# Kernel optimization log

Measured on AMD Instinct MI355X. Metric: run time of the kernel, lower is better.

Reference implementation:

```python
import jax, jax.numpy as jnp
import numpy as np

PERIOD = 64
SCALE = 0.45


def setup_inputs() -> dict:
    key = jax.random.key(0)
    kq, kk, kv = jax.random.split(key, 3)
    B, L, D = 16, 8192, 512
    q = jax.random.normal(kq, (B, L, D), dtype=jnp.float32)
    k = jax.random.normal(kk, (B, L, D), dtype=jnp.float32)
    v = jax.random.normal(kv, (B, L, D), dtype=jnp.float32)
    return {"q": q, "k": k, "v": v}


def reference(q, k, v):
    # q, k, v: [B, L, D] with L % PERIOD == 0 and L == S, so the padding /
    # length-matching branches of the torch module are no-ops.
    B, L, D = q.shape
    nblk = L // PERIOD
    # permute to [B, D, L] then chunk the sequence into blocks of size PERIOD:
    # [B, D, nblk, PERIOD]. Attention is computed ACROSS blocks, with the
    # period dimension acting as the feature dimension.
    qb = q.transpose(0, 2, 1).reshape(B, D, nblk, PERIOD)
    kb = k.transpose(0, 2, 1).reshape(B, D, nblk, PERIOD)
    vb = v.transpose(0, 2, 1).reshape(B, D, nblk, PERIOD)
    # attn: [B, D, nblk, nblk]
    attn = jax.nn.softmax(jnp.einsum('bdnp,bdmp->bdnm', qb, kb) * SCALE, axis=-1)
    # out: [B, D, nblk, PERIOD] -> [B, D, L] -> [B, L, D]
    out = jnp.einsum('bdnm,bdmp->bdnp', attn, vb)
    out = out.reshape(B, D, L).transpose(0, 2, 1)
    return (out, attn)
```

## Files before the change

kernel.cpp:

```cpp
#include <hip/hip_runtime.h>
#include <stdint.h>

#define BB 16
#define LSEQ 8192
#define DD 512
#define PER 64
#define NBLK 128
#define QSCALE 0.45f

typedef __attribute__((ext_vector_type(8))) short short8;
typedef __attribute__((ext_vector_type(4))) float f32x4;
typedef __attribute__((ext_vector_type(2))) unsigned int uint2v;
typedef unsigned short ushort_t;

__device__ __forceinline__ ushort_t f2bf(float f) {
    union { float f; uint32_t u; } c; c.f = f;
    uint32_t u = c.u + 0x7FFFu + ((c.u >> 16) & 1u);
    return (ushort_t)(u >> 16);
}
__device__ __forceinline__ float bf2f(ushort_t h) {
    union { float f; uint32_t u; } c; c.u = ((uint32_t)h) << 16;
    return c.f;
}
__device__ __forceinline__ uint32_t pk2(float a, float b) {
    return (uint32_t)f2bf(a) | ((uint32_t)f2bf(b) << 16);
}

__global__ __launch_bounds__(256) void kt1(const float* __restrict__ q,
                                           const float* __restrict__ k,
                                           ushort_t* __restrict__ qT,
                                           ushort_t* __restrict__ kT) {
    const int t = threadIdx.x;
    const int zz = blockIdx.z;
    const int b = zz & (BB - 1);
    const bool isk = zz >= BB;
    const float scale = isk ? 1.0f : QSCALE;
    const float* sp = (isk ? k : q) + (size_t)b * LSEQ * DD;
    ushort_t* dp = (isk ? kT : qT) + (size_t)b * DD * LSEQ;
    const int l0 = blockIdx.x * 64 + 4 * (t & 15);
    const int d0 = blockIdx.y * 64 + 4 * (t >> 4);
    f32x4 v[4];
#pragma unroll
    for (int j = 0; j < 4; ++j)
        v[j] = __builtin_nontemporal_load(
            (const f32x4*)(sp + (size_t)(l0 + j) * DD + d0));
#pragma unroll
    for (int dj = 0; dj < 4; ++dj) {
        uint2v w;
        w[0] = pk2(v[0][dj] * scale, v[1][dj] * scale);
        w[1] = pk2(v[2][dj] * scale, v[3][dj] * scale);
        *(uint2v*)(dp + (size_t)(d0 + dj) * LSEQ + l0) = w;
    }
}

__global__ __launch_bounds__(256) void kt2(const float* __restrict__ v,
                                           ushort_t* __restrict__ vtt) {
    const int t = threadIdx.x;
    const int p  = blockIdx.x & 63;
    const int mh = blockIdx.x >> 6;
    const int m0 = mh * 64 + 4 * (t & 15);
    const int d0 = blockIdx.y * 64 + 4 * (t >> 4);
    const int b = blockIdx.z;
    const float* vp = v + (size_t)b * LSEQ * DD;
    f32x4 x[4];
#pragma unroll
    for (int mj = 0; mj < 4; ++mj)
        x[mj] = __builtin_nontemporal_load(
            (const f32x4*)(vp + (size_t)((m0 + mj) * PER + p) * DD + d0));
#pragma unroll
    for (int dj = 0; dj < 4; ++dj) {
        uint2v w;
        w[0] = pk2(x[0][dj], x[1][dj]);
        w[1] = pk2(x[2][dj], x[3][dj]);
        *(uint2v*)(vtt + (size_t)((size_t)(b * DD + d0 + dj) * PER + p) * NBLK + m0) = w;
    }
}

__global__ __launch_bounds__(256) void katt(const ushort_t* __restrict__ qT,
                                            const ushort_t* __restrict__ kT,
                                            const ushort_t* __restrict__ vTT,
                                            float* __restrict__ attn,
                                            ushort_t* __restrict__ outT) {
    __shared__ __align__(16) ushort_t sm[40960];
    ushort_t* Qs = sm;
    ushort_t* Ks = sm + 8192;
    ushort_t* Vs = sm + 16384;
    ushort_t* Ps = sm + 24576;

    const int t = threadIdx.x;
    const int bd = blockIdx.x;
    const size_t base = (size_t)bd * 8192;
    const ushort_t* qp = qT + base;
    const ushort_t* kp = kT + base;
    const ushort_t* vp = vTT + base;

#pragma unroll
    for (int it = 0; it < 4; ++it) {
        int e = it * 2048 + t * 8;
        int n = e >> 6, pc = (e >> 3) & 7;
        int gq = pc ^ (n & 7);
        *(short8*)&Qs[n * 64 + gq * 8] = __builtin_nontemporal_load((const short8*)(qp + e));
        *(short8*)&Ks[n * 64 + gq * 8] = __builtin_nontemporal_load((const short8*)(kp + e));
        int p = e >> 7, mc = (e >> 3) & 15;
        int gv = mc ^ (p & 7);
        *(short8*)&Vs[p * 128 + gv * 8] = __builtin_nontemporal_load((const short8*)(vp + e));
    }
    __syncthreads();

    const int lane = t & 63, w = t >> 6;
    const int lrow = lane & 15, lquad = lane >> 4;

    f32x4 acc[2][8];
#pragma unroll
    for (int nt = 0; nt < 2; ++nt)
#pragma unroll
        for (int mt = 0; mt < 8; ++mt) acc[nt][mt] = (f32x4){0.f, 0.f, 0.f, 0.f};

    short8 aQ[2][2];
#pragma unroll
    for (int nt = 0; nt < 2; ++nt) {
        int n = w * 32 + nt * 16 + lrow;
#pragma unroll
        for (int s = 0; s < 2; ++s) {
            int g = (s * 4 + lquad) ^ (n & 7);
            aQ[nt][s] = *(const short8*)&Qs[n * 64 + g * 8];
        }
    }
#pragma unroll
    for (int mt = 0; mt < 8; ++mt) {
        int m = mt * 16 + lrow;
#pragma unroll
        for (int s = 0; s < 2; ++s) {
            int g = (s * 4 + lquad) ^ (m & 7);
            short8 bK = *(const short8*)&Ks[m * 64 + g * 8];
#pragma unroll
            for (int nt = 0; nt < 2; ++nt)
                acc[nt][mt] = __builtin_amdgcn_mfma_f32_16x16x32_bf16(aQ[nt][s], bK, acc[nt][mt], 0, 0, 0);
        }
    }

    float* attnp = attn + (size_t)bd * (NBLK * NBLK);
#pragma unroll
    for (int nt = 0; nt < 2; ++nt) {
        int nbase = w * 32 + nt * 16;
#pragma unroll
        for (int r = 0; r < 4; ++r) {
            int row = nbase + lquad * 4 + r;
            float pv[8];
            float mx = -1e30f;
#pragma unroll
            for (int mt = 0; mt < 8; ++mt) { pv[mt] = acc[nt][mt][r]; mx = fmaxf(mx, pv[mt]); }
#pragma unroll
            for (int msk = 1; msk < 16; msk <<= 1) mx = fmaxf(mx, __shfl_xor(mx, msk, 64));
            float sum = 0.f;
#pragma unroll
            for (int mt = 0; mt < 8; ++mt) {
                pv[mt] = exp2f((pv[mt] - mx) * 1.4426950408889634f);
                sum += pv[mt];
            }
#pragma unroll
            for (int msk = 1; msk < 16; msk <<= 1) sum += __shfl_xor(sum, msk, 64);
            float inv = 1.0f / sum;
#pragma unroll
            for (int mt = 0; mt < 8; ++mt) {
                float a = pv[mt] * inv;
                int m = mt * 16 + lrow;
                __builtin_nontemporal_store(a, attnp + (size_t)row * NBLK + m);
                int g = (m >> 3) ^ (row & 7);
                Ps[row * 128 + g * 8 + (m & 7)] = f2bf(a);
            }
        }
    }

    f32x4 oacc[2][4];
#pragma unroll
    for (int nt = 0; nt < 2; ++nt)
#pragma unroll
        for (int pt = 0; pt < 4; ++pt) oacc[nt][pt] = (f32x4){0.f, 0.f, 0.f, 0.f};

#pragma unroll
    for (int s = 0; s < 4; ++s) {
        short8 aP[2];
#pragma unroll
        for (int nt = 0; nt < 2; ++nt) {
            int n = w * 32 + nt * 16 + lrow;
            int g = (s * 4 + lquad) ^ (n & 7);
            aP[nt] = *(const short8*)&Ps[n * 128 + g * 8];
        }
#pragma unroll
        for (int pt = 0; pt < 4; ++pt) {
            int prow = pt * 16 + lrow;
            int gv = (s * 4 + lquad) ^ (prow & 7);
            short8 bV = *(const short8*)&Vs[prow * 128 + gv * 8];
#pragma unroll
            for (int nt = 0; nt < 2; ++nt)
                oacc[nt][pt] = __builtin_amdgcn_mfma_f32_16x16x32_bf16(aP[nt], bV, oacc[nt][pt], 0, 0, 0);
        }
    }

    ushort_t* op = outT + base;
#pragma unroll
    for (int nt = 0; nt < 2; ++nt)
#pragma unroll
        for (int pt = 0; pt < 4; ++pt)
#pragma unroll
            for (int r = 0; r < 4; ++r) {
                int row = w * 32 + nt * 16 + lquad * 4 + r;
                int p = pt * 16 + lrow;
                op[row * PER + p] = f2bf(oacc[nt][pt][r]);
            }
}

__global__ __launch_bounds__(256) void ko(const ushort_t* __restrict__ outT,
                                          float* __restrict__ out) {
    const int t = threadIdx.x;
    const int l0 = blockIdx.x * 64 + 4 * (t & 15);
    const int d0 = blockIdx.y * 64 + 4 * (t >> 4);
    const int b = blockIdx.z;
    const ushort_t* sp = outT + (size_t)b * DD * LSEQ;
    float* op = out + (size_t)b * LSEQ * DD;
    uint2v ld[4];
#pragma unroll
    for (int dd = 0; dd < 4; ++dd)
        ld[dd] = __builtin_nontemporal_load(
            (const uint2v*)(sp + (size_t)(d0 + dd) * LSEQ + l0));
#pragma unroll
    for (int j = 0; j < 4; ++j) {
        f32x4 o;
#pragma unroll
        for (int dd = 0; dd < 4; ++dd)
            o[dd] = bf2f((ushort_t)((ld[dd][j >> 1] >> ((j & 1) * 16)) & 0xffffu));
        __builtin_nontemporal_store(o, (f32x4*)(op + (size_t)(l0 + j) * DD + d0));
    }
}

extern "C" void kernel_launch(void* const* d_in, const int* in_sizes, int n_in,
                              void* d_out, int out_size, void* d_ws, size_t ws_size,
                              hipStream_t stream) {
    const float* q = (const float*)d_in[0];
    const float* k = (const float*)d_in[1];
    const float* v = (const float*)d_in[2];
    float* outp = (float*)d_out;
    float* attnp = outp + (size_t)BB * LSEQ * DD;

    ushort_t* qT  = (ushort_t*)d_ws;
    ushort_t* kT  = qT  + (size_t)BB * DD * LSEQ;
    ushort_t* vTT = kT  + (size_t)BB * DD * LSEQ;
    ushort_t* oT  = vTT + (size_t)BB * DD * LSEQ;

    dim3 g1(LSEQ / 64, DD / 64, BB * 2);
    kt1<<<g1, 256, 0, stream>>>(q, k, qT, kT);
    dim3 g2(2 * PER, DD / 64, BB);
    kt2<<<g2, 256, 0, stream>>>(v, vTT);
    katt<<<dim3(BB * DD), 256, 0, stream>>>(qT, kT, vTT, attnp, oT);
    dim3 g3(LSEQ / 64, DD / 64, BB);
    ko<<<g3, 256, 0, stream>>>(oT, outp);
}
```

Measured before the change: 511.9 us.

## Merge transpose kernels and alias P buffer over Q/K in shared memory

```diff
diff --git a/kernel.cpp b/kernel.cpp
--- a/kernel.cpp
+++ b/kernel.cpp
@@ -26,66 +26,65 @@
     return (uint32_t)f2bf(a) | ((uint32_t)f2bf(b) << 16);
 }
 
-__global__ __launch_bounds__(256) void kt1(const float* __restrict__ q,
+__global__ __launch_bounds__(256) void ktr(const float* __restrict__ q,
                                            const float* __restrict__ k,
+                                           const float* __restrict__ v,
                                            ushort_t* __restrict__ qT,
-                                           ushort_t* __restrict__ kT) {
+                                           ushort_t* __restrict__ kT,
+                                           ushort_t* __restrict__ vTT) {
     const int t = threadIdx.x;
     const int zz = blockIdx.z;
+    const int role = zz >> 4;
     const int b = zz & (BB - 1);
-    const bool isk = zz >= BB;
-    const float scale = isk ? 1.0f : QSCALE;
-    const float* sp = (isk ? k : q) + (size_t)b * LSEQ * DD;
-    ushort_t* dp = (isk ? kT : qT) + (size_t)b * DD * LSEQ;
-    const int l0 = blockIdx.x * 64 + 4 * (t & 15);
-    const int d0 = blockIdx.y * 64 + 4 * (t >> 4);
-    f32x4 v[4];
-#pragma unroll
-    for (int j = 0; j < 4; ++j)
-        v[j] = __builtin_nontemporal_load(
-            (const f32x4*)(sp + (size_t)(l0 + j) * DD + d0));
-#pragma unroll
-    for (int dj = 0; dj < 4; ++dj) {
-        uint2v w;
-        w[0] = pk2(v[0][dj] * scale, v[1][dj] * scale);
-        w[1] = pk2(v[2][dj] * scale, v[3][dj] * scale);
-        *(uint2v*)(dp + (size_t)(d0 + dj) * LSEQ + l0) = w;
-    }
-}
-
-__global__ __launch_bounds__(256) void kt2(const float* __restrict__ v,
-                                           ushort_t* __restrict__ vtt) {
-    const int t = threadIdx.x;
-    const int p  = blockIdx.x & 63;
-    const int mh = blockIdx.x >> 6;
-    const int m0 = mh * 64 + 4 * (t & 15);
-    const int d0 = blockIdx.y * 64 + 4 * (t >> 4);
-    const int b = blockIdx.z;
-    const float* vp = v + (size_t)b * LSEQ * DD;
-    f32x4 x[4];
-#pragma unroll
-    for (int mj = 0; mj < 4; ++mj)
-        x[mj] = __builtin_nontemporal_load(
-            (const f32x4*)(vp + (size_t)((m0 + mj) * PER + p) * DD + d0));
-#pragma unroll
-    for (int dj = 0; dj < 4; ++dj) {
-        uint2v w;
-        w[0] = pk2(x[0][dj], x[1][dj]);
-        w[1] = pk2(x[2][dj], x[3][dj]);
-        *(uint2v*)(vtt + (size_t)((size_t)(b * DD + d0 + dj) * PER + p) * NBLK + m0) = w;
-    }
-}
-
-__global__ __launch_bounds__(256) void katt(const ushort_t* __restrict__ qT,
-                                            const ushort_t* __restrict__ kT,
-                                            const ushort_t* __restrict__ vTT,
-                                            float* __restrict__ attn,
-                                            ushort_t* __restrict__ outT) {
-    __shared__ __align__(16) ushort_t sm[40960];
+    if (role < 2) {
+        const float scale = role ? 1.0f : QSCALE;
+        const float* sp = (role ? k : q) + (size_t)b * LSEQ * DD;
+        ushort_t* dp = (role ? kT : qT) + (size_t)b * DD * LSEQ;
+        const int l0 = blockIdx.x * 64 + 4 * (t & 15);
+        const int d0 = blockIdx.y * 64 + 4 * (t >> 4);
+        f32x4 vv[4];
+#pragma unroll
+        for (int j = 0; j < 4; ++j)
+            vv[j] = __builtin_nontemporal_load(
+                (const f32x4*)(sp + (size_t)(l0 + j) * DD + d0));
+#pragma unroll
+        for (int dj = 0; dj < 4; ++dj) {
+            uint2v w;
+            w[0] = pk2(vv[0][dj] * scale, vv[1][dj] * scale);
+            w[1] = pk2(vv[2][dj] * scale, vv[3][dj] * scale);
+            *(uint2v*)(dp + (size_t)(d0 + dj) * LSEQ + l0) = w;
+        }
+    } else {
+        const int p = blockIdx.x & 63;
+        const int mh = blockIdx.x >> 6;
+        const int m0 = mh * 64 + 4 * (t & 15);
+        const int d0 = blockIdx.y * 64 + 4 * (t >> 4);
+        const float* vp = v + (size_t)b * LSEQ * DD;
+        f32x4 x[4];
+#pragma unroll
+        for (int mj = 0; mj < 4; ++mj)
+            x[mj] = __builtin_nontemporal_load(
+                (const f32x4*)(vp + (size_t)((m0 + mj) * PER + p) * DD + d0));
+#pragma unroll
+        for (int dj = 0; dj < 4; ++dj) {
+            uint2v w;
+            w[0] = pk2(x[0][dj], x[1][dj]);
+            w[1] = pk2(x[2][dj], x[3][dj]);
+            *(uint2v*)(vTT + (size_t)((size_t)(b * DD + d0 + dj) * PER + p) * NBLK + m0) = w;
+        }
+    }
+}
+
+__global__ __launch_bounds__(256, 3) void katt(const ushort_t* __restrict__ qT,
+                                               const ushort_t* __restrict__ kT,
+                                               const ushort_t* __restrict__ vTT,
+                                               float* __restrict__ attn,
+                                               ushort_t* __restrict__ outT) {
+    __shared__ __align__(16) ushort_t sm[24576];
     ushort_t* Qs = sm;
     ushort_t* Ks = sm + 8192;
+    ushort_t* Ps = sm;
     ushort_t* Vs = sm + 16384;
-    ushort_t* Ps = sm + 24576;
 
     const int t = threadIdx.x;
     const int bd = blockIdx.x;
@@ -138,6 +137,7 @@
                 acc[nt][mt] = __builtin_amdgcn_mfma_f32_16x16x32_bf16(aQ[nt][s], bK, acc[nt][mt], 0, 0, 0);
         }
     }
+    __syncthreads();
 
     float* attnp = attn + (size_t)bd * (NBLK * NBLK);
 #pragma unroll
@@ -248,10 +248,8 @@
     ushort_t* vTT = kT  + (size_t)BB * DD * LSEQ;
     ushort_t* oT  = vTT + (size_t)BB * DD * LSEQ;
 
-    dim3 g1(LSEQ / 64, DD / 64, BB * 2);
-    kt1<<<g1, 256, 0, stream>>>(q, k, qT, kT);
-    dim3 g2(2 * PER, DD / 64, BB);
-    kt2<<<g2, 256, 0, stream>>>(v, vTT);
+    dim3 g1(LSEQ / 64, DD / 64, BB * 3);
+    ktr<<<g1, 256, 0, stream>>>(q, k, v, qT, kT, vTT);
     katt<<<dim3(BB * DD), 256, 0, stream>>>(qT, kT, vTT, attnp, oT);
     dim3 g3(LSEQ / 64, DD / 64, BB);
     ko<<<g3, 256, 0, stream>>>(oT, outp);
```

Measured after the change: 494.3 us. 3.4% less time.
